# Kernel optimization log

Measured on AMD Instinct MI355X. Metric: run time of the kernel, lower is better.

## Reference

```python
import jax, jax.numpy as jnp
import numpy as np

K = 8                    # batch_k: images per class
MARGIN = 0.2
NU = 0.0
CUTOFF = 0.5
NONZERO_LOSS_CUTOFF = 1.4
EPS = 1e-8


def setup_inputs() -> dict:
    key = jax.random.key(0)
    k1, k2 = jax.random.split(key)
    n, d = 8192, 128
    x = jax.random.normal(k1, (n, d), dtype=jnp.float32)
    # unit-norm embeddings (paper assumption; keeps distances < 2 so
    # log(1 - 0.25*d^2) in the sampling weights stays finite)
    x = x / jnp.linalg.norm(x, axis=1, keepdims=True)
    y = jax.random.randint(k2, (n,), 0, 1024, dtype=jnp.int64)
    beta_in = jnp.ones((n,), dtype=jnp.float32)
    return {"x": x, "y": y, "beta_in": beta_in}


def _sampling(x, key):
    """Distance-weighted sampling. Returns (a_index, p_index, n_index),
    each of length n*(K-1). Mirrors the numpy/CPU sampling loop."""
    x = jax.lax.stop_gradient(x)        # torch code samples on detached features
    n, d = x.shape
    sq = jnp.sum(x * x, axis=1, keepdims=True)            # [n,1]
    dist2 = sq + sq.T - 2.0 * (x @ x.T)                    # [n,n]
    dist = jnp.sqrt(dist2 + jnp.eye(n, dtype=x.dtype))     # diag -> 1, as in original
    dist = jnp.maximum(dist, CUTOFF)
    # log q(d) ~ (2-d)*log(dist) - (d-3)/2 * log(1 - dist^2/4)
    log_w = (2.0 - d) * jnp.log(dist) - (d - 3) / 2.0 * jnp.log(1.0 - 0.25 * dist * dist)
    w = jnp.exp(log_w - jnp.max(log_w))
    block = jnp.arange(n) // K
    mask = (block[:, None] != block[None, :]) & (dist < NONZERO_LOSS_CUTOFF)
    w = w * mask
    row_ok = jnp.sum(w, axis=1) > 0.0
    # categorical logits: log of weights (row-normalization is irrelevant to
    # categorical sampling); fallback to uniform for degenerate rows, matching
    # the original's try/except np.random.choice fallback.
    logits = jnp.where(w > 0.0, jnp.log(w + 1e-30), -jnp.inf)
    logits = jnp.where(row_ok[:, None], logits, 0.0)
    n_index = jax.random.categorical(key, logits, shape=(K - 1, n)).T.reshape(-1)  # [n*(K-1)]

    # anchors: each i repeated K-1 times; positives: the other K-1 members of
    # i's block, in block order (self pushed last by stable argsort on bool)
    idx = jnp.arange(n)
    a_index = jnp.repeat(idx, K - 1)
    cand = (idx // K * K)[:, None] + jnp.arange(K)[None, :]        # [n,K]
    order = jnp.argsort(cand == idx[:, None], axis=1, stable=True)
    p_index = jnp.take_along_axis(cand, order, axis=1)[:, : K - 1].reshape(-1)
    return a_index, p_index, n_index


def reference(x, y, beta_in):
    a_index, p_index, n_index = _sampling(x, jax.random.key(42))
    beta_work = beta_in[a_index]
    beta_reg_loss = jnp.sum(beta_work) * NU
    anchors = x[a_index]
    positives = x[p_index]
    negatives = x[n_index]
    d_ap = jnp.sqrt(jnp.sum((anchors - positives) ** 2, axis=1) + EPS)
    d_an = jnp.sqrt(jnp.sum((anchors - negatives) ** 2, axis=1) + EPS)
    pos_loss = jax.nn.relu(d_ap - beta_work + MARGIN)
    neg_loss = jax.nn.relu(beta_work - d_an + MARGIN)
    pair_cnt = jnp.sum((pos_loss > 0.0).astype(jnp.float32) + (neg_loss > 0.0).astype(jnp.float32))
    loss = (jnp.sum(pos_loss + neg_loss) + beta_reg_loss) / pair_cnt
    return loss
```

## Files before the change

### kernel.cpp

```cpp
#include <hip/hip_runtime.h>
#include <math.h>


#define NROWS 8192
#define DDIM  128
#define NPAIRF 7.0f
#define BT 128
#define NTILE (NROWS / BT)
#define NPAIRS (NTILE * (NTILE + 1) / 2)
#define LW2_SHIFT 57.70780163555852f
#define FINAL_BLOCKS 256

typedef short bf16x8 __attribute__((ext_vector_type(8)));
typedef float f32x4  __attribute__((ext_vector_type(4)));

template <bool B> struct BoolK { static constexpr bool value = B; };

__device__ __forceinline__ unsigned short f2bf(float f) {
    unsigned int u = __float_as_uint(f);
    return (unsigned short)((u + 0x7fffu + ((u >> 16) & 1u)) >> 16);
}

__device__ __forceinline__ void stage_from_x(const float* __restrict__ x,
        int base_row, unsigned short* buf, int tid) {
#pragma unroll
    for (int t = 0; t < 8; t++) {
        int s = tid + t * 256;
        int row = s >> 4;
        int kb = s & 15;
        int phys = row * 16 + (kb ^ (row & 7));
        const float4* src = (const float4*)&x[(size_t)(base_row + row) * DDIM + kb * 8];
        float4 v0 = src[0], v1 = src[1];
        uint4 pk;
        pk.x = (unsigned)f2bf(v0.x) | ((unsigned)f2bf(v0.y) << 16);
        pk.y = (unsigned)f2bf(v0.z) | ((unsigned)f2bf(v0.w) << 16);
        pk.z = (unsigned)f2bf(v1.x) | ((unsigned)f2bf(v1.y) << 16);
        pk.w = (unsigned)f2bf(v1.z) | ((unsigned)f2bf(v1.w) << 16);
        ((uint4*)buf)[phys] = pk;
    }
}

__global__ void prep_kernel(float* __restrict__ rowacc, float* __restrict__ accum) {
    int t = blockIdx.x * 256 + threadIdx.x;
    if (t < NROWS * 3) rowacc[t] = 0.0f;
    if (t < 8) accum[t] = 0.0f;
}

template <bool DET>
__global__ __launch_bounds__(256, 2) void gram_kernel(
        const float* __restrict__ x, const float* __restrict__ beta,
        float* __restrict__ Pout, float* __restrict__ accum) {
    __shared__ unsigned short Abuf[BT * DDIM];
    __shared__ unsigned short Bbuf[BT * DDIM];
    __shared__ float comb_rows[BT][3];
    __shared__ float comb_cols[BT][3];

    if (DET && blockIdx.x == 0 && threadIdx.x == 0) accum[2] = 0.0f;

    int rem = blockIdx.x, I = 0;
    while (rem >= NTILE - I) { rem -= NTILE - I; ++I; }
    const int J = I + rem;
    const int row0 = I * BT, col0 = J * BT;

    const int tid = threadIdx.x;
    const int lane = tid & 63;
    const int wave = tid >> 6;
    const int wy = wave >> 1, wx = wave & 1;
    const int l15 = lane & 15, quad = lane >> 4;

    stage_from_x(x, row0, Abuf, tid);
    stage_from_x(x, col0, Bbuf, tid);

    f32x4 acc[4][4];
#pragma unroll
    for (int i = 0; i < 4; i++)
#pragma unroll
        for (int j = 0; j < 4; j++) acc[i][j] = (f32x4){0.f, 0.f, 0.f, 0.f};

    __syncthreads();

#pragma unroll
    for (int kc = 0; kc < 4; kc++) {
        bf16x8 af[4], bfr[4];
#pragma unroll
        for (int i = 0; i < 4; i++) {
            int ra = wy * 64 + i * 16 + l15;
            int pa = (kc * 4 + quad) ^ (ra & 7);
            af[i] = *(const bf16x8*)&Abuf[(ra * 16 + pa) * 8];
            int rb = wx * 64 + i * 16 + l15;
            int pb = (kc * 4 + quad) ^ (rb & 7);
            bfr[i] = *(const bf16x8*)&Bbuf[(rb * 16 + pb) * 8];
        }
#pragma unroll
        for (int i = 0; i < 4; i++)
#pragma unroll
            for (int j = 0; j < 4; j++)
                acc[i][j] = __builtin_amdgcn_mfma_f32_16x16x32_bf16(
                    af[i], bfr[j], acc[i][j], 0, 0, 0);
    }

    float bpc4[4];
    int cloc4[4];
#pragma unroll
    for (int j = 0; j < 4; j++) {
        int cl = wx * 64 + j * 16 + l15;
        bpc4[j] = beta[col0 + cl] + 0.2f;
        cloc4[j] = cl >> 3;
    }
    float bpm16[16];
    int rloc16[16];
#pragma unroll
    for (int i = 0; i < 4; i++)
#pragma unroll
        for (int reg = 0; reg < 4; reg++) {
            int idx = i * 4 + reg;
            int rl = wy * 64 + i * 16 + quad * 4 + reg;
            bpm16[idx] = beta[row0 + rl] + 0.2f;
            rloc16[idx] = rl >> 3;
        }

    float ts0[16], ts1[16], ts2[16];
    float tc0[4], tc1[4], tc2[4];
#pragma unroll
    for (int k = 0; k < 16; k++) ts0[k] = ts1[k] = ts2[k] = 0.0f;
#pragma unroll
    for (int k = 0; k < 4; k++) tc0[k] = tc1[k] = tc2[k] = 0.0f;

    auto fold = [&](auto diag_c) {
        constexpr bool DIAG = decltype(diag_c)::value;
#pragma unroll
        for (int i = 0; i < 4; i++)
#pragma unroll
            for (int reg = 0; reg < 4; reg++) {
                const int idx = i * 4 + reg;
                const float bpm = bpm16[idx];
#pragma unroll
                for (int j = 0; j < 4; j++) {
                    float g = acc[i][j][reg];
                    float dist2 = fmaxf(fmaf(-2.0f, g, 2.0f), 0.0f);
                    float d = __builtin_amdgcn_sqrtf(dist2 + 1e-8f);
                    float t = fmaxf(dist2, 0.25f);
                    float u = fmaf(-0.25f, t, 1.0f);
                    float lw2 = fmaf(-63.0f, __builtin_amdgcn_logf(t),
                                fmaf(-62.5f, __builtin_amdgcn_logf(u), -LW2_SHIFT));
                    bool valid = t < 1.96f;
                    if (DIAG) valid = valid && (rloc16[idx] != cloc4[j]);
                    float w = valid ? __builtin_amdgcn_exp2f(lw2) : 0.0f;
                    float nlr = fmaxf(bpm - d, 0.0f);
                    ts0[idx] += w;
                    ts1[idx] = fmaf(w, nlr, ts1[idx]);
                    ts2[idx] += (nlr > 0.0f) ? w : 0.0f;
                    if (!DIAG) {
                        float nlc = fmaxf(bpc4[j] - d, 0.0f);
                        tc0[j] += w;
                        tc1[j] = fmaf(w, nlc, tc1[j]);
                        tc2[j] += (nlc > 0.0f) ? w : 0.0f;
                    }
                }
            }
    };
    if (I == J) fold(BoolK<true>{}); else fold(BoolK<false>{});

    float r0 = 0.f, r1 = 0.f, r2 = 0.f;
#pragma unroll
    for (int idx = 0; idx < 16; idx++) {
        float t0 = ts0[idx], t1 = ts1[idx], t2 = ts2[idx];
#pragma unroll
        for (int off = 1; off < 16; off <<= 1) {
            t0 += __shfl_xor(t0, off);
            t1 += __shfl_xor(t1, off);
            t2 += __shfl_xor(t2, off);
        }
        if (l15 == idx) { r0 = t0; r1 = t1; r2 = t2; }
    }
    const int rowl = wy * 64 + (l15 >> 2) * 16 + quad * 4 + (l15 & 3);

    float c0 = 0.f, c1 = 0.f, c2 = 0.f;
#pragma unroll
    for (int j = 0; j < 4; j++) {
        float t0 = tc0[j], t1 = tc1[j], t2 = tc2[j];
        t0 += __shfl_xor(t0, 16); t1 += __shfl_xor(t1, 16); t2 += __shfl_xor(t2, 16);
        t0 += __shfl_xor(t0, 32); t1 += __shfl_xor(t1, 32); t2 += __shfl_xor(t2, 32);
        if (quad == j) { c0 = t0; c1 = t1; c2 = t2; }
    }
    const int coll = wx * 64 + quad * 16 + l15;

    if (wx == 0) {
        comb_rows[rowl][0] = r0; comb_rows[rowl][1] = r1; comb_rows[rowl][2] = r2;
    }
    if (wy == 0 && I != J) {
        comb_cols[coll][0] = c0; comb_cols[coll][1] = c1; comb_cols[coll][2] = c2;
    }
    __syncthreads();
    if (wx == 1) {
        float v0 = r0 + comb_rows[rowl][0];
        float v1 = r1 + comb_rows[rowl][1];
        float v2 = r2 + comb_rows[rowl][2];
        int rg = row0 + rowl;
        if (DET) {
            Pout[(0 * NTILE + J) * NROWS + rg] = v0;
            Pout[(1 * NTILE + J) * NROWS + rg] = v1;
            Pout[(2 * NTILE + J) * NROWS + rg] = v2;
        } else {
            atomicAdd(&Pout[rg * 3 + 0], v0);
            atomicAdd(&Pout[rg * 3 + 1], v1);
            atomicAdd(&Pout[rg * 3 + 2], v2);
        }
    }
    if (wy == 1 && I != J) {
        float v0 = c0 + comb_cols[coll][0];
        float v1 = c1 + comb_cols[coll][1];
        float v2 = c2 + comb_cols[coll][2];
        int cg = col0 + coll;
        if (DET) {
            Pout[(0 * NTILE + I) * NROWS + cg] = v0;
            Pout[(1 * NTILE + I) * NROWS + cg] = v1;
            Pout[(2 * NTILE + I) * NROWS + cg] = v2;
        } else {
            atomicAdd(&Pout[cg * 3 + 0], v0);
            atomicAdd(&Pout[cg * 3 + 1], v1);
            atomicAdd(&Pout[cg * 3 + 2], v2);
        }
    }
}

template <bool DET>
__global__ __launch_bounds__(256) void final_kernel(
        const float* __restrict__ x, const float* __restrict__ beta,
        const float* __restrict__ Pin, float* __restrict__ accum,
        float* __restrict__ blkpart, float* __restrict__ out) {
    __shared__ float sm[8];
    __shared__ bool amLast;
    const int tid = threadIdx.x;
    int t = blockIdx.x * 256 + tid;
    int i = t >> 3;
    int p = t & 7;
    int j = (i & ~7) + p;
    float betai = beta[i];
    const float4* xi = (const float4*)&x[(size_t)i * DDIM];
    const float4* xj = (const float4*)&x[(size_t)j * DDIM];
    float d2 = 0.0f;
#pragma unroll
    for (int k = 0; k < DDIM / 4; k++) {
        float4 va = xi[k], vb = xj[k];
        float dx = va.x - vb.x, dy = va.y - vb.y;
        float dz = va.z - vb.z, dw = va.w - vb.w;
        d2 = fmaf(dx, dx, fmaf(dy, dy, fmaf(dz, dz, fmaf(dw, dw, d2))));
    }
    float d = __builtin_amdgcn_sqrtf(d2 + 1e-8f);
    float nl = fmaxf(betai - d + 0.2f, 0.0f);
    float fb1 = nl;
    float fb2 = (nl > 0.0f) ? 1.0f : 0.0f;
    float num = 0.f, cnt = 0.f;
    if (j != i) {
        float pl = fmaxf(d - betai + 0.2f, 0.0f);
        num = pl;
        cnt = (pl > 0.0f) ? 1.0f : 0.0f;
    }
    float a0 = 0.f, a1 = 0.f, a2 = 0.f;
    if (DET) {
#pragma unroll
        for (int k = 0; k < 8; k++) {
            int s = p + k * 8;
            a0 += Pin[(0 * NTILE + s) * NROWS + i];
            a1 += Pin[(1 * NTILE + s) * NROWS + i];
            a2 += Pin[(2 * NTILE + s) * NROWS + i];
        }
    }
#pragma unroll
    for (int off = 1; off < 8; off <<= 1) {
        num += __shfl_xor(num, off); cnt += __shfl_xor(cnt, off);
        fb1 += __shfl_xor(fb1, off); fb2 += __shfl_xor(fb2, off);
        a0 += __shfl_xor(a0, off);  a1 += __shfl_xor(a1, off);
        a2 += __shfl_xor(a2, off);
    }
    if (p == 0) {
        if (!DET) { a0 = Pin[i * 3 + 0]; a1 = Pin[i * 3 + 1]; a2 = Pin[i * 3 + 2]; }
        if (a0 > 0.0f) {
            num += NPAIRF * a1 / a0;
            cnt += NPAIRF * a2 / a0;
        } else {
            num += NPAIRF * fb1 / (float)NROWS;
            cnt += NPAIRF * fb2 / (float)NROWS;
        }
    } else {
        num = 0.f; cnt = 0.f;
    }
#pragma unroll
    for (int off = 8; off < 64; off <<= 1) {
        num += __shfl_xor(num, off);
        cnt += __shfl_xor(cnt, off);
    }
    int wv = tid >> 6, ln = tid & 63;
    if (ln == 0) { sm[wv] = num; sm[4 + wv] = cnt; }
    __syncthreads();
    if (tid == 0) {
        float n2 = 0.f, c2 = 0.f;
#pragma unroll
        for (int w = 0; w < 4; w++) { n2 += sm[w]; c2 += sm[4 + w]; }
        blkpart[blockIdx.x * 2 + 0] = n2;
        blkpart[blockIdx.x * 2 + 1] = c2;
        __threadfence();
        amLast = (atomicAdd(&accum[2], 1.0f) == (float)(gridDim.x - 1));
    }
    __syncthreads();
    if (amLast) {
        __threadfence();
        float n = blkpart[tid * 2 + 0];
        float c = blkpart[tid * 2 + 1];
#pragma unroll
        for (int off = 1; off < 64; off <<= 1) {
            n += __shfl_xor(n, off);
            c += __shfl_xor(c, off);
        }
        if (ln == 0) { sm[wv] = n; sm[4 + wv] = c; }
        __syncthreads();
        if (tid == 0) {
            float nn = 0.f, cc = 0.f;
#pragma unroll
            for (int w = 0; w < 4; w++) { nn += sm[w]; cc += sm[4 + w]; }
            out[0] = nn / cc;
            accum[2] = 0.0f;
        }
    }
}

extern "C" void kernel_launch(void* const* d_in, const int* in_sizes, int n_in,
                              void* d_out, int out_size, void* d_ws, size_t ws_size,
                              hipStream_t stream) {
    const float* x = (const float*)d_in[0];
    const float* beta = (const float*)d_in[2];
    float* out = (float*)d_out;
    float* ws = (float*)d_ws;

    float* accum = ws;
    float* blkpart = ws + 64;
    float* P = blkpart + FINAL_BLOCKS * 2;

    const size_t det_bytes = (64 + FINAL_BLOCKS * 2
                              + (size_t)3 * NTILE * NROWS) * 4;
    if (ws_size >= det_bytes) {
        gram_kernel<true><<<NPAIRS, 256, 0, stream>>>(x, beta, P, accum);
        final_kernel<true><<<FINAL_BLOCKS, 256, 0, stream>>>(x, beta, P, accum,
                                                             blkpart, out);
    } else {
        float* rowacc = blkpart + FINAL_BLOCKS * 2;
        prep_kernel<<<(NROWS * 3 + 255) / 256, 256, 0, stream>>>(rowacc, accum);
        gram_kernel<false><<<NPAIRS, 256, 0, stream>>>(x, beta, rowacc, accum);
        final_kernel<false><<<FINAL_BLOCKS, 256, 0, stream>>>(x, beta, rowacc, accum,
                                                              blkpart, out);
    }
}
```

Baseline: 131.5 us.

## Double gram block to 512 threads with 32x64 wave tiles and LDS atomic reduction

The gram kernel now runs 8 waves per block instead of 4. Each wave computes a 32x64 sub-tile, which halves the accumulators and per-thread row state. Row and column partial sums are merged with shared-memory atomics into zero-initialised comb buffers, then written out by the first 256 threads. The aim is more resident waves to hide the latency of the transcendental-heavy fold, at the cost of redundant B-fragment LDS reads, more column shuffle reductions, and LDS atomic contention.

```diff
diff --git a/kernel.cpp b/kernel.cpp
--- a/kernel.cpp
+++ b/kernel.cpp
@@ -24,8 +24,8 @@
 __device__ __forceinline__ void stage_from_x(const float* __restrict__ x,
         int base_row, unsigned short* buf, int tid) {
 #pragma unroll
-    for (int t = 0; t < 8; t++) {
-        int s = tid + t * 256;
+    for (int t = 0; t < 4; t++) {
+        int s = tid + t * 512;
         int row = s >> 4;
         int kb = s & 15;
         int phys = row * 16 + (kb ^ (row & 7));
@@ -47,7 +47,7 @@
 }
 
 template <bool DET>
-__global__ __launch_bounds__(256, 2) void gram_kernel(
+__global__ __launch_bounds__(512) void gram_kernel(
         const float* __restrict__ x, const float* __restrict__ beta,
         float* __restrict__ Pout, float* __restrict__ accum) {
     __shared__ unsigned short Abuf[BT * DDIM];
@@ -68,12 +68,19 @@
     const int wy = wave >> 1, wx = wave & 1;
     const int l15 = lane & 15, quad = lane >> 4;
 
+    if (tid < BT) {
+        comb_rows[tid][0] = comb_rows[tid][1] = comb_rows[tid][2] = 0.0f;
+    } else if (tid < 2 * BT) {
+        int c = tid - BT;
+        comb_cols[c][0] = comb_cols[c][1] = comb_cols[c][2] = 0.0f;
+    }
+
     stage_from_x(x, row0, Abuf, tid);
     stage_from_x(x, col0, Bbuf, tid);
 
-    f32x4 acc[4][4];
-#pragma unroll
-    for (int i = 0; i < 4; i++)
+    f32x4 acc[2][4];
+#pragma unroll
+    for (int i = 0; i < 2; i++)
 #pragma unroll
         for (int j = 0; j < 4; j++) acc[i][j] = (f32x4){0.f, 0.f, 0.f, 0.f};
 
@@ -81,22 +88,23 @@
 
 #pragma unroll
     for (int kc = 0; kc < 4; kc++) {
-        bf16x8 af[4], bfr[4];
-#pragma unroll
-        for (int i = 0; i < 4; i++) {
-            int ra = wy * 64 + i * 16 + l15;
+        bf16x8 bfr[4];
+#pragma unroll
+        for (int j = 0; j < 4; j++) {
+            int rb = wx * 64 + j * 16 + l15;
+            int pb = (kc * 4 + quad) ^ (rb & 7);
+            bfr[j] = *(const bf16x8*)&Bbuf[(rb * 16 + pb) * 8];
+        }
+#pragma unroll
+        for (int i = 0; i < 2; i++) {
+            int ra = wy * 32 + i * 16 + l15;
             int pa = (kc * 4 + quad) ^ (ra & 7);
-            af[i] = *(const bf16x8*)&Abuf[(ra * 16 + pa) * 8];
-            int rb = wx * 64 + i * 16 + l15;
-            int pb = (kc * 4 + quad) ^ (rb & 7);
-            bfr[i] = *(const bf16x8*)&Bbuf[(rb * 16 + pb) * 8];
-        }
-#pragma unroll
-        for (int i = 0; i < 4; i++)
+            bf16x8 af = *(const bf16x8*)&Abuf[(ra * 16 + pa) * 8];
 #pragma unroll
             for (int j = 0; j < 4; j++)
                 acc[i][j] = __builtin_amdgcn_mfma_f32_16x16x32_bf16(
-                    af[i], bfr[j], acc[i][j], 0, 0, 0);
+                    af, bfr[j], acc[i][j], 0, 0, 0);
+        }
     }
 
     float bpc4[4];
@@ -107,33 +115,33 @@
         bpc4[j] = beta[col0 + cl] + 0.2f;
         cloc4[j] = cl >> 3;
     }
-    float bpm16[16];
-    int rloc16[16];
-#pragma unroll
-    for (int i = 0; i < 4; i++)
+    float bpm8[8];
+    int rloc8[8];
+#pragma unroll
+    for (int i = 0; i < 2; i++)
 #pragma unroll
         for (int reg = 0; reg < 4; reg++) {
             int idx = i * 4 + reg;
-            int rl = wy * 64 + i * 16 + quad * 4 + reg;
-            bpm16[idx] = beta[row0 + rl] + 0.2f;
-            rloc16[idx] = rl >> 3;
-        }
-
-    float ts0[16], ts1[16], ts2[16];
+            int rl = wy * 32 + i * 16 + quad * 4 + reg;
+            bpm8[idx] = beta[row0 + rl] + 0.2f;
+            rloc8[idx] = rl >> 3;
+        }
+
+    float ts0[8], ts1[8], ts2[8];
     float tc0[4], tc1[4], tc2[4];
 #pragma unroll
-    for (int k = 0; k < 16; k++) ts0[k] = ts1[k] = ts2[k] = 0.0f;
+    for (int k = 0; k < 8; k++) ts0[k] = ts1[k] = ts2[k] = 0.0f;
 #pragma unroll
     for (int k = 0; k < 4; k++) tc0[k] = tc1[k] = tc2[k] = 0.0f;
 
     auto fold = [&](auto diag_c) {
         constexpr bool DIAG = decltype(diag_c)::value;
 #pragma unroll
-        for (int i = 0; i < 4; i++)
+        for (int i = 0; i < 2; i++)
 #pragma unroll
             for (int reg = 0; reg < 4; reg++) {
                 const int idx = i * 4 + reg;
-                const float bpm = bpm16[idx];
+                const float bpm = bpm8[idx];
 #pragma unroll
                 for (int j = 0; j < 4; j++) {
                     float g = acc[i][j][reg];
@@ -144,7 +152,7 @@
                     float lw2 = fmaf(-63.0f, __builtin_amdgcn_logf(t),
                                 fmaf(-62.5f, __builtin_amdgcn_logf(u), -LW2_SHIFT));
                     bool valid = t < 1.96f;
-                    if (DIAG) valid = valid && (rloc16[idx] != cloc4[j]);
+                    if (DIAG) valid = valid && (rloc8[idx] != cloc4[j]);
                     float w = valid ? __builtin_amdgcn_exp2f(lw2) : 0.0f;
                     float nlr = fmaxf(bpm - d, 0.0f);
                     ts0[idx] += w;
@@ -163,7 +171,7 @@
 
     float r0 = 0.f, r1 = 0.f, r2 = 0.f;
 #pragma unroll
-    for (int idx = 0; idx < 16; idx++) {
+    for (int idx = 0; idx < 8; idx++) {
         float t0 = ts0[idx], t1 = ts1[idx], t2 = ts2[idx];
 #pragma unroll
         for (int off = 1; off < 16; off <<= 1) {
@@ -173,53 +181,51 @@
         }
         if (l15 == idx) { r0 = t0; r1 = t1; r2 = t2; }
     }
-    const int rowl = wy * 64 + (l15 >> 2) * 16 + quad * 4 + (l15 & 3);
-
-    float c0 = 0.f, c1 = 0.f, c2 = 0.f;
-#pragma unroll
-    for (int j = 0; j < 4; j++) {
-        float t0 = tc0[j], t1 = tc1[j], t2 = tc2[j];
-        t0 += __shfl_xor(t0, 16); t1 += __shfl_xor(t1, 16); t2 += __shfl_xor(t2, 16);
-        t0 += __shfl_xor(t0, 32); t1 += __shfl_xor(t1, 32); t2 += __shfl_xor(t2, 32);
-        if (quad == j) { c0 = t0; c1 = t1; c2 = t2; }
-    }
-    const int coll = wx * 64 + quad * 16 + l15;
-
-    if (wx == 0) {
-        comb_rows[rowl][0] = r0; comb_rows[rowl][1] = r1; comb_rows[rowl][2] = r2;
-    }
-    if (wy == 0 && I != J) {
-        comb_cols[coll][0] = c0; comb_cols[coll][1] = c1; comb_cols[coll][2] = c2;
+    if (l15 < 8) {
+        int rowl = wy * 32 + (l15 >> 2) * 16 + quad * 4 + (l15 & 3);
+        atomicAdd(&comb_rows[rowl][0], r0);
+        atomicAdd(&comb_rows[rowl][1], r1);
+        atomicAdd(&comb_rows[rowl][2], r2);
+    }
+
+    if (I != J) {
+        float c0 = 0.f, c1 = 0.f, c2 = 0.f;
+#pragma unroll
+        for (int j = 0; j < 4; j++) {
+            float t0 = tc0[j], t1 = tc1[j], t2 = tc2[j];
+            t0 += __shfl_xor(t0, 16); t1 += __shfl_xor(t1, 16); t2 += __shfl_xor(t2, 16);
+            t0 += __shfl_xor(t0, 32); t1 += __shfl_xor(t1, 32); t2 += __shfl_xor(t2, 32);
+            if (quad == j) { c0 = t0; c1 = t1; c2 = t2; }
+        }
+        int coll = wx * 64 + quad * 16 + l15;
+        atomicAdd(&comb_cols[coll][0], c0);
+        atomicAdd(&comb_cols[coll][1], c1);
+        atomicAdd(&comb_cols[coll][2], c2);
     }
     __syncthreads();
-    if (wx == 1) {
-        float v0 = r0 + comb_rows[rowl][0];
-        float v1 = r1 + comb_rows[rowl][1];
-        float v2 = r2 + comb_rows[rowl][2];
-        int rg = row0 + rowl;
+
+    if (tid < BT) {
+        int rg = row0 + tid;
         if (DET) {
-            Pout[(0 * NTILE + J) * NROWS + rg] = v0;
-            Pout[(1 * NTILE + J) * NROWS + rg] = v1;
-            Pout[(2 * NTILE + J) * NROWS + rg] = v2;
+            Pout[(0 * NTILE + J) * NROWS + rg] = comb_rows[tid][0];
+            Pout[(1 * NTILE + J) * NROWS + rg] = comb_rows[tid][1];
+            Pout[(2 * NTILE + J) * NROWS + rg] = comb_rows[tid][2];
         } else {
-            atomicAdd(&Pout[rg * 3 + 0], v0);
-            atomicAdd(&Pout[rg * 3 + 1], v1);
-            atomicAdd(&Pout[rg * 3 + 2], v2);
-        }
-    }
-    if (wy == 1 && I != J) {
-        float v0 = c0 + comb_cols[coll][0];
-        float v1 = c1 + comb_cols[coll][1];
-        float v2 = c2 + comb_cols[coll][2];
-        int cg = col0 + coll;
+            atomicAdd(&Pout[rg * 3 + 0], comb_rows[tid][0]);
+            atomicAdd(&Pout[rg * 3 + 1], comb_rows[tid][1]);
+            atomicAdd(&Pout[rg * 3 + 2], comb_rows[tid][2]);
+        }
+    } else if (tid < 2 * BT && I != J) {
+        int c = tid - BT;
+        int cg = col0 + c;
         if (DET) {
-            Pout[(0 * NTILE + I) * NROWS + cg] = v0;
-            Pout[(1 * NTILE + I) * NROWS + cg] = v1;
-            Pout[(2 * NTILE + I) * NROWS + cg] = v2;
+            Pout[(0 * NTILE + I) * NROWS + cg] = comb_cols[c][0];
+            Pout[(1 * NTILE + I) * NROWS + cg] = comb_cols[c][1];
+            Pout[(2 * NTILE + I) * NROWS + cg] = comb_cols[c][2];
         } else {
-            atomicAdd(&Pout[cg * 3 + 0], v0);
-            atomicAdd(&Pout[cg * 3 + 1], v1);
-            atomicAdd(&Pout[cg * 3 + 2], v2);
+            atomicAdd(&Pout[cg * 3 + 0], comb_cols[c][0]);
+            atomicAdd(&Pout[cg * 3 + 1], comb_cols[c][1]);
+            atomicAdd(&Pout[cg * 3 + 2], comb_cols[c][2]);
         }
     }
 }
@@ -340,13 +346,13 @@
     const size_t det_bytes = (64 + FINAL_BLOCKS * 2
                               + (size_t)3 * NTILE * NROWS) * 4;
     if (ws_size >= det_bytes) {
-        gram_kernel<true><<<NPAIRS, 256, 0, stream>>>(x, beta, P, accum);
+        gram_kernel<true><<<NPAIRS, 512, 0, stream>>>(x, beta, P, accum);
         final_kernel<true><<<FINAL_BLOCKS, 256, 0, stream>>>(x, beta, P, accum,
                                                              blkpart, out);
     } else {
         float* rowacc = blkpart + FINAL_BLOCKS * 2;
         prep_kernel<<<(NROWS * 3 + 255) / 256, 256, 0, stream>>>(rowacc, accum);
-        gram_kernel<false><<<NPAIRS, 256, 0, stream>>>(x, beta, rowacc, accum);
+        gram_kernel<false><<<NPAIRS, 512, 0, stream>>>(x, beta, rowacc, accum);
         final_kernel<false><<<FINAL_BLOCKS, 256, 0, stream>>>(x, beta, rowacc, accum,
                                                               blkpart, out);
     }
```

New measurement: 167.7 us. +27.5%, slower.

## Stage gram tiles in K-halves to cut LDS and drop launch-bound occupancy hint

Applied to the files above, without the earlier changes.

Splits the shared-memory staging of the A and B tiles into two 64-wide K halves, reusing half-size LDS buffers with an extra barrier between halves. This halves LDS use per block, which can allow more resident blocks. It also removes the min-blocks-per-CU launch bound, which frees the compiler's register budget, and folds the clamp and epsilon add in the distance calculation into fewer instructions. The cost is serialized load and compute phases with extra syncs, and possibly lower occupancy if register use grows.

```diff
diff --git a/kernel.cpp b/kernel.cpp
--- a/kernel.cpp
+++ b/kernel.cpp
@@ -21,15 +21,16 @@
     return (unsigned short)((u + 0x7fffu + ((u >> 16) & 1u)) >> 16);
 }
 
-__device__ __forceinline__ void stage_from_x(const float* __restrict__ x,
-        int base_row, unsigned short* buf, int tid) {
-#pragma unroll
-    for (int t = 0; t < 8; t++) {
+__device__ __forceinline__ void stage_half(const float* __restrict__ x,
+        int base_row, int kh, unsigned short* buf, int tid) {
+#pragma unroll
+    for (int t = 0; t < 4; t++) {
         int s = tid + t * 256;
-        int row = s >> 4;
-        int kb = s & 15;
-        int phys = row * 16 + (kb ^ (row & 7));
-        const float4* src = (const float4*)&x[(size_t)(base_row + row) * DDIM + kb * 8];
+        int row = s >> 3;
+        int kb = s & 7;
+        int phys = row * 8 + (kb ^ (row & 7));
+        const float4* src =
+            (const float4*)&x[(size_t)(base_row + row) * DDIM + kh * 64 + kb * 8];
         float4 v0 = src[0], v1 = src[1];
         uint4 pk;
         pk.x = (unsigned)f2bf(v0.x) | ((unsigned)f2bf(v0.y) << 16);
@@ -47,11 +48,11 @@
 }
 
 template <bool DET>
-__global__ __launch_bounds__(256, 2) void gram_kernel(
+__global__ __launch_bounds__(256) void gram_kernel(
         const float* __restrict__ x, const float* __restrict__ beta,
         float* __restrict__ Pout, float* __restrict__ accum) {
-    __shared__ unsigned short Abuf[BT * DDIM];
-    __shared__ unsigned short Bbuf[BT * DDIM];
+    __shared__ unsigned short Abuf[BT * 64];
+    __shared__ unsigned short Bbuf[BT * 64];
     __shared__ float comb_rows[BT][3];
     __shared__ float comb_cols[BT][3];
 
@@ -68,35 +69,38 @@
     const int wy = wave >> 1, wx = wave & 1;
     const int l15 = lane & 15, quad = lane >> 4;
 
-    stage_from_x(x, row0, Abuf, tid);
-    stage_from_x(x, col0, Bbuf, tid);
-
     f32x4 acc[4][4];
 #pragma unroll
     for (int i = 0; i < 4; i++)
 #pragma unroll
         for (int j = 0; j < 4; j++) acc[i][j] = (f32x4){0.f, 0.f, 0.f, 0.f};
 
-    __syncthreads();
-
-#pragma unroll
-    for (int kc = 0; kc < 4; kc++) {
-        bf16x8 af[4], bfr[4];
-#pragma unroll
-        for (int i = 0; i < 4; i++) {
-            int ra = wy * 64 + i * 16 + l15;
-            int pa = (kc * 4 + quad) ^ (ra & 7);
-            af[i] = *(const bf16x8*)&Abuf[(ra * 16 + pa) * 8];
-            int rb = wx * 64 + i * 16 + l15;
-            int pb = (kc * 4 + quad) ^ (rb & 7);
-            bfr[i] = *(const bf16x8*)&Bbuf[(rb * 16 + pb) * 8];
-        }
-#pragma unroll
-        for (int i = 0; i < 4; i++)
-#pragma unroll
-            for (int j = 0; j < 4; j++)
-                acc[i][j] = __builtin_amdgcn_mfma_f32_16x16x32_bf16(
-                    af[i], bfr[j], acc[i][j], 0, 0, 0);
+#pragma unroll
+    for (int kh = 0; kh < 2; kh++) {
+        if (kh) __syncthreads();
+        stage_half(x, row0, kh, Abuf, tid);
+        stage_half(x, col0, kh, Bbuf, tid);
+        __syncthreads();
+
+#pragma unroll
+        for (int kcl = 0; kcl < 2; kcl++) {
+            bf16x8 af[4], bfr[4];
+#pragma unroll
+            for (int i = 0; i < 4; i++) {
+                int ra = wy * 64 + i * 16 + l15;
+                int pa = (kcl * 4 + quad) ^ (ra & 7);
+                af[i] = *(const bf16x8*)&Abuf[(ra * 8 + pa) * 8];
+                int rb = wx * 64 + i * 16 + l15;
+                int pb = (kcl * 4 + quad) ^ (rb & 7);
+                bfr[i] = *(const bf16x8*)&Bbuf[(rb * 8 + pb) * 8];
+            }
+#pragma unroll
+            for (int i = 0; i < 4; i++)
+#pragma unroll
+                for (int j = 0; j < 4; j++)
+                    acc[i][j] = __builtin_amdgcn_mfma_f32_16x16x32_bf16(
+                        af[i], bfr[j], acc[i][j], 0, 0, 0);
+        }
     }
 
     float bpc4[4];
@@ -137,9 +141,9 @@
 #pragma unroll
                 for (int j = 0; j < 4; j++) {
                     float g = acc[i][j][reg];
-                    float dist2 = fmaxf(fmaf(-2.0f, g, 2.0f), 0.0f);
-                    float d = __builtin_amdgcn_sqrtf(dist2 + 1e-8f);
-                    float t = fmaxf(dist2, 0.25f);
+                    float base = fmaf(-2.0f, g, 2.0f);
+                    float d = __builtin_amdgcn_sqrtf(fmaxf(base, 1e-8f));
+                    float t = fmaxf(base, 0.25f);
                     float u = fmaf(-0.25f, t, 1.0f);
                     float lw2 = fmaf(-63.0f, __builtin_amdgcn_logf(t),
                                 fmaf(-62.5f, __builtin_amdgcn_logf(u), -LW2_SHIFT));
```

Measured after the change: 155.9 us. +18.5%, slower.
